# Kernel tuning notes

Hardware: AMD Instinct MI355X
Metric: run time of the kernel (lower is better)

## Reference

```python
import jax, jax.numpy as jnp
import numpy as np

N_HEAD = 16
LN_EPS = 1e-5


def _layernorm(x, g, b):
    mu = jnp.mean(x, axis=-1, keepdims=True)
    var = jnp.var(x, axis=-1, keepdims=True)
    return (x - mu) * jax.lax.rsqrt(var + LN_EPS) * g + b


def setup_inputs() -> dict:
    key = jax.random.key(0)
    ks = jax.random.split(key, 8)
    B, T, C = 8, 1024, 1024
    s = lambda fan_in: 1.0 / np.sqrt(fan_in)
    return {
        "x": jax.random.normal(ks[0], (B, T, C), jnp.float32),
        "kqv_w": jax.random.normal(ks[1], (3 * C, C), jnp.float32) * s(C),
        "kqv_b": jnp.zeros((3 * C,), jnp.float32),
        "proj_w": jax.random.normal(ks[2], (C, C), jnp.float32) * s(C),
        "proj_b": jnp.zeros((C,), jnp.float32),
        "ln1_g": jnp.ones((C,), jnp.float32),
        "ln1_b": jnp.zeros((C,), jnp.float32),
        "ln2_g": jnp.ones((C,), jnp.float32),
        "ln2_b": jnp.zeros((C,), jnp.float32),
        "fc1_w": jax.random.normal(ks[3], (4 * C, C), jnp.float32) * s(C),
        "fc1_b": jnp.zeros((4 * C,), jnp.float32),
        "fc2_w": jax.random.normal(ks[4], (C, 4 * C), jnp.float32) * s(4 * C),
        "fc2_b": jnp.zeros((C,), jnp.float32),
    }


def reference(x, kqv_w, kqv_b, proj_w, proj_b, ln1_g, ln1_b, ln2_g, ln2_b,
              fc1_w, fc1_b, fc2_w, fc2_b):
    B, T, C = x.shape
    hd = C // N_HEAD

    # --- attention sublayer ---
    h = _layernorm(x, ln1_g, ln1_b)
    kqv = h @ kqv_w.T + kqv_b                     # [B,T,3C]
    kqv = kqv.reshape(B, T, N_HEAD, 3 * hd)
    # ts.slice(kqv, 3, dim=-1) -> (k, q, v) in that order
    k = kqv[..., 0 * hd:1 * hd].transpose(0, 2, 1, 3)  # [B,H,T,hd]
    q = kqv[..., 1 * hd:2 * hd].transpose(0, 2, 1, 3)
    v = kqv[..., 2 * hd:3 * hd].transpose(0, 2, 1, 3)

    att = jnp.einsum('bhqd,bhkd->bhqk', q, k) * (1.0 / np.sqrt(hd))
    causal = jnp.tril(jnp.ones((T, T), dtype=bool))
    att = jnp.where(causal, att, jnp.float32(-jnp.inf))
    att = jax.nn.softmax(att, axis=-1)
    y = jnp.einsum('bhqk,bhkd->bhqd', att, v)     # [B,H,T,hd]
    y = y.transpose(0, 2, 1, 3).reshape(B, T, C)
    x = x + (y @ proj_w.T + proj_b)

    # --- MLP sublayer ---
    h = _layernorm(x, ln2_g, ln2_b)
    h = jax.nn.gelu(h @ fc1_w.T + fc1_b, approximate=False)  # nn.GELU exact
    x = x + (h @ fc2_w.T + fc2_b)
    return x
```

## Files before the change

### kernel.cpp

```cpp
#include <hip/hip_runtime.h>
#include <math.h>
#include <stdint.h>

typedef __bf16 bf16_t;
typedef __bf16 bf16x8 __attribute__((ext_vector_type(8)));
typedef float f32x4 __attribute__((ext_vector_type(4)));
typedef unsigned short ushort8_t __attribute__((ext_vector_type(8)));
typedef unsigned short ushort4_t __attribute__((ext_vector_type(4)));

#define LOG2E 1.44269504088896340736f

__device__ inline unsigned short f2bf_bits(float f) {
  union { float f; unsigned int u; } v; v.f = f;
  unsigned int u = v.u;
  return (unsigned short)((u + 0x7fffu + ((u >> 16) & 1u)) >> 16);
}

__device__ inline void gld_lds16(const void* g, void* l) {
  __builtin_amdgcn_global_load_lds(
      (__attribute__((address_space(1))) void*)(uintptr_t)(g),
      (__attribute__((address_space(3))) void*)(uintptr_t)(l),
      16, 0, 0);
}

#define BAR() __builtin_amdgcn_s_barrier()
#define LGKM0() asm volatile("s_waitcnt lgkmcnt(0)" ::: "memory")
#define VMW(n) asm volatile("s_waitcnt vmcnt(" #n ")" ::: "memory")
#define PRIO(p) __builtin_amdgcn_s_setprio(p)

__global__ __launch_bounds__(256) void cast_kernel(const float* __restrict__ in,
                                                   unsigned short* __restrict__ out,
                                                   int n) {
  int i = (blockIdx.x * 256 + threadIdx.x) * 4;
  if (i >= n) return;
  float4 f = *reinterpret_cast<const float4*>(in + i);
  ushort4_t o;
  o[0] = f2bf_bits(f.x); o[1] = f2bf_bits(f.y);
  o[2] = f2bf_bits(f.z); o[3] = f2bf_bits(f.w);
  *reinterpret_cast<ushort4_t*>(out + i) = o;
}

__global__ __launch_bounds__(256) void ln_kernel(const float* __restrict__ x,
                                                 const float* __restrict__ g,
                                                 const float* __restrict__ bta,
                                                 unsigned short* __restrict__ out) {
  const int row = blockIdx.x;
  const int c = threadIdx.x * 4;
  const float4 xv = *reinterpret_cast<const float4*>(x + (size_t)row * 1024 + c);
  float s = xv.x + xv.y + xv.z + xv.w;
  float sq = xv.x * xv.x + xv.y * xv.y + xv.z * xv.z + xv.w * xv.w;
#pragma unroll
  for (int xm = 1; xm < 64; xm <<= 1) {
    s += __shfl_xor(s, xm, 64);
    sq += __shfl_xor(sq, xm, 64);
  }
  __shared__ float sh[8];
  const int wave = threadIdx.x >> 6, lane = threadIdx.x & 63;
  if (lane == 0) { sh[wave] = s; sh[4 + wave] = sq; }
  __syncthreads();
  const float ts = sh[0] + sh[1] + sh[2] + sh[3];
  const float tq = sh[4] + sh[5] + sh[6] + sh[7];
  const float mean = ts * (1.0f / 1024.0f);
  const float var = tq * (1.0f / 1024.0f) - mean * mean;
  const float rstd = rsqrtf(var + 1e-5f);
  const float4 gv = *reinterpret_cast<const float4*>(g + c);
  const float4 bv = *reinterpret_cast<const float4*>(bta + c);
  ushort4_t o;
  o[0] = f2bf_bits((xv.x - mean) * rstd * gv.x + bv.x);
  o[1] = f2bf_bits((xv.y - mean) * rstd * gv.y + bv.y);
  o[2] = f2bf_bits((xv.z - mean) * rstd * gv.z + bv.z);
  o[3] = f2bf_bits((xv.w - mean) * rstd * gv.w + bv.w);
  *reinterpret_cast<ushort4_t*>(out + (size_t)row * 1024 + c) = o;
}

#define LDAF(SLOT)                                                            \
  do {                                                                        \
    _Pragma("unroll") for (int mi_ = 0; mi_ < 4; ++mi_)                       \
    _Pragma("unroll") for (int kh_ = 0; kh_ < 2; ++kh_) {                     \
      const int row_ = wm * 64 + mi_ * 16 + lr16;                             \
      af[mi_][kh_] = *reinterpret_cast<const bf16x8*>(                        \
          &lds[(SLOT) * AS + row_ * 64 + ((kh_ * 32 + lk * 8) ^ axor)]);      \
    }                                                                         \
  } while (0)

#define LDBF(SLOT, HALF)                                                      \
  do {                                                                        \
    _Pragma("unroll") for (int n2_ = 0; n2_ < 2; ++n2_)                       \
    _Pragma("unroll") for (int kh_ = 0; kh_ < 2; ++kh_) {                     \
      const int row_ = wn * 64 + ((HALF) * 2 + n2_) * 16 + lr16;              \
      bf[n2_][kh_] = *reinterpret_cast<const bf16x8*>(                        \
          &lds[BS0 + (SLOT) * BSS + row_ * 64 + ((kh_ * 32 + lk * 8) ^ axor)]); \
    }                                                                         \
  } while (0)

#define PMMA(HALF)                                                            \
  do {                                                                        \
    _Pragma("unroll") for (int mi_ = 0; mi_ < 4; ++mi_)                       \
    _Pragma("unroll") for (int n2_ = 0; n2_ < 2; ++n2_)                       \
    _Pragma("unroll") for (int kh_ = 0; kh_ < 2; ++kh_)                       \
      acc[mi_][(HALF) * 2 + n2_] = __builtin_amdgcn_mfma_f32_16x16x32_bf16(   \
          af[mi_][kh_], bf[n2_][kh_], acc[mi_][(HALF) * 2 + n2_], 0, 0, 0);   \
  } while (0)

template <int EPI>
__global__ __launch_bounds__(512) void gemm8(const unsigned short* __restrict__ A,
                                             const unsigned short* __restrict__ W,
                                             const float* __restrict__ bias,
                                             const float* __restrict__ res,
                                             unsigned short* __restrict__ outb,
                                             float* __restrict__ outf,
                                             int N, int K) {
  __shared__ unsigned short lds[(2 * 128 + 2 * 256) * 64];
  const int tid = threadIdx.x;
  const int w = tid >> 6, l = tid & 63;
  const int m0 = blockIdx.y * 128, n0 = blockIdx.x * 256;
  const int wm = w >> 2, wn = w & 3;
  const int lr16 = l & 15, lk = l >> 4;
  const int axor = (lr16 & 7) << 3;

  const int AS = 128 * 64;
  const int BS0 = 2 * 128 * 64;
  const int BSS = 256 * 64;

  const int sr = tid >> 3;
  const int sx = ((tid & 7) ^ (sr & 7)) << 3;
  auto stA = [&](int t, int h) {
    gld_lds16(A + (size_t)(m0 + h * 64 + sr) * K + t * 64 + sx,
              &lds[(t & 1) * AS + h * 4096 + tid * 8]);
  };
  auto stB = [&](int t, int c) {
    gld_lds16(W + (size_t)(n0 + c * 64 + sr) * K + t * 64 + sx,
              &lds[BS0 + (t & 1) * BSS + c * 4096 + tid * 8]);
  };

  f32x4 acc[4][4];
#pragma unroll
  for (int i = 0; i < 4; ++i)
#pragma unroll
    for (int j = 0; j < 4; ++j) { f32x4 z = {0.f, 0.f, 0.f, 0.f}; acc[i][j] = z; }
  bf16x8 af[4][2], bf[2][2];

  stA(0, 0); stA(0, 1);
  stB(0, 0); stB(0, 1); stB(0, 2); stB(0, 3);
  stA(1, 0); stA(1, 1);
  VMW(2);
  BAR();

  const int nt = K / 64;
  for (int e = 0; e < nt; e += 2) {
    const int o = e + 1;
    const int e2 = (e + 2 < nt) ? (e + 2) : 0;
    const int o2 = (e + 3 < nt) ? (e + 3) : 1;

    LDAF(0); LDBF(0, 0);
    stB(o, 0); stB(o, 1); stB(o, 2); stB(o, 3);
    BAR(); LGKM0(); PRIO(1); PMMA(0); PRIO(0); BAR();
    LDBF(0, 1);
    stA(e2, 0); stA(e2, 1);
    BAR(); LGKM0(); PRIO(1); PMMA(1); PRIO(0);
    VMW(2);
    BAR();
    LDAF(1); LDBF(1, 0);
    stB(e2, 0); stB(e2, 1); stB(e2, 2); stB(e2, 3);
    BAR(); LGKM0(); PRIO(1); PMMA(0); PRIO(0); BAR();
    LDBF(1, 1);
    stA(o2, 0); stA(o2, 1);
    BAR(); LGKM0(); PRIO(1); PMMA(1); PRIO(0);
    VMW(2);
    BAR();
  }
  VMW(0);

#pragma unroll
  for (int ni = 0; ni < 4; ++ni) {
    const int col = n0 + wn * 64 + ni * 16 + lr16;
    const float bv = bias[col];
#pragma unroll
    for (int mi = 0; mi < 4; ++mi) {
#pragma unroll
      for (int r = 0; r < 4; ++r) {
        const int row = m0 + wm * 64 + mi * 16 + lk * 4 + r;
        const size_t idx = (size_t)row * N + col;
        float v = acc[mi][ni][r] + bv;
        if (EPI == 0) {
          outb[idx] = f2bf_bits(v);
        } else if (EPI == 1) {
          outf[idx] = v + res[idx];
        } else {
          v = 0.5f * v * (1.0f + erff(v * 0.70710678118654752f));
          outb[idx] = f2bf_bits(v);
        }
      }
    }
  }
}

__device__ inline int swz(int row, int colelem) {
  return row * 64 + (colelem ^ ((row & 7) << 3));
}

__global__ __launch_bounds__(256) void attn_kernel(const unsigned short* __restrict__ kqv,
                                                   unsigned short* __restrict__ y) {
  __shared__ unsigned short Ks[2][64 * 64];
  __shared__ unsigned short Vt[2][64 * 64];
  __shared__ unsigned short Ps[4][16 * 64];

  const int tid = threadIdx.x;
  const int wave = tid >> 6;
  const int lane = tid & 63;
  const int bh = blockIdx.x;
  const int pair = blockIdx.y;
  const int b = bh >> 4;
  const int h = bh & 15;
  const int lo = pair;
  const int hi = 15 - pair;
  const int bT = b * 1024;
  const int hoff = h * 192;

  auto loadq = [&](int q0t, bf16x8 (&qf)[2]) {
    const unsigned short* qp =
        kqv + (size_t)(bT + q0t + wave * 16 + (lane & 15)) * 3072 + hoff + 64 +
        (lane >> 4) * 8;
#pragma unroll
    for (int kk = 0; kk < 2; ++kk) {
      bf16x8 t = *reinterpret_cast<const bf16x8*>(qp + kk * 32);
#pragma unroll
      for (int e = 0; e < 8; ++e) t[e] = (bf16_t)((float)t[e] * 0.125f);
      qf[kk] = t;
    }
  };

  auto stageK = [&](int j0, int bufi) {
#pragma unroll
    for (int i = 0; i < 2; ++i) {
      const int off = i * 4096 + wave * 1024 + lane * 16;
      const int jr = off >> 7;
      const int ce = ((off & 127) >> 1) ^ ((jr & 7) << 3);
      gld_lds16(kqv + (size_t)(bT + j0 + jr) * 3072 + hoff + ce,
                &Ks[bufi][i * 2048 + wave * 512]);
    }
  };

  ushort8_t vreg0, vreg1;
  auto vload = [&](int j0) {
    const unsigned short* vp =
        kqv + (size_t)(bT + j0 + (tid & 63)) * 3072 + hoff + 128 + (tid >> 6) * 8;
    vreg0 = *reinterpret_cast<const ushort8_t*>(vp);
    vreg1 = *reinterpret_cast<const ushort8_t*>(vp + 32);
  };
  auto vwrite = [&](int bufi) {
    const int j = tid & 63;
    const int dg = tid >> 6;
#pragma unroll
    for (int e = 0; e < 8; ++e) Vt[bufi][swz(dg * 8 + e, j)] = vreg0[e];
#pragma unroll
    for (int e = 0; e < 8; ++e) Vt[bufi][swz((dg + 4) * 8 + e, j)] = vreg1[e];
  };

  auto compute = [&](const bf16x8 (&qf)[2], f32x4 (&acc_o)[4], float (&mr)[4],
                     float (&lr)[4], int q0t, int j0, bool diag, int cur) {
    f32x4 s[4];
#pragma unroll
    for (int nt = 0; nt < 4; ++nt) {
      f32x4 a = {0.f, 0.f, 0.f, 0.f};
#pragma unroll
      for (int kk = 0; kk < 2; ++kk) {
        const bf16x8 kf = *reinterpret_cast<const bf16x8*>(
            &Ks[cur][swz(nt * 16 + (lane & 15), kk * 32 + (lane >> 4) * 8)]);
        a = __builtin_amdgcn_mfma_f32_16x16x32_bf16(qf[kk], kf, a, 0, 0, 0);
      }
      s[nt] = a;
    }
#pragma unroll
    for (int r = 0; r < 4; ++r) {
      float mx = -1e30f;
      if (diag) {
        const int qg = q0t + wave * 16 + ((lane >> 4) << 2) + r;
#pragma unroll
        for (int nt = 0; nt < 4; ++nt) {
          const int jg = j0 + nt * 16 + (lane & 15);
          const float sv = (jg <= qg) ? s[nt][r] : -1e30f;
          s[nt][r] = sv;
          mx = fmaxf(mx, sv);
        }
      } else {
#pragma unroll
        for (int nt = 0; nt < 4; ++nt) mx = fmaxf(mx, s[nt][r]);
      }
#pragma unroll
      for (int xm = 1; xm < 16; xm <<= 1) mx = fmaxf(mx, __shfl_xor(mx, xm, 64));
      const float mnew = fmaxf(mr[r], mx);
      const float sc = exp2f((mr[r] - mnew) * LOG2E);
      mr[r] = mnew;
      float ssum = 0.f;
#pragma unroll
      for (int nt = 0; nt < 4; ++nt) {
        const float p = exp2f((s[nt][r] - mnew) * LOG2E);
        s[nt][r] = p;
        ssum += p;
      }
#pragma unroll
      for (int xm = 1; xm < 16; xm <<= 1) ssum += __shfl_xor(ssum, xm, 64);
      lr[r] = lr[r] * sc + ssum;
#pragma unroll
      for (int dt = 0; dt < 4; ++dt) acc_o[dt][r] *= sc;
    }
    unsigned short* Pw = &Ps[wave][0];
#pragma unroll
    for (int nt = 0; nt < 4; ++nt)
#pragma unroll
      for (int r = 0; r < 4; ++r)
        Pw[swz(((lane >> 4) << 2) + r, nt * 16 + (lane & 15))] = f2bf_bits(s[nt][r]);
#pragma unroll
    for (int kk = 0; kk < 2; ++kk) {
      const bf16x8 pf = *reinterpret_cast<const bf16x8*>(
          &Ps[wave][swz(lane & 15, kk * 32 + (lane >> 4) * 8)]);
#pragma unroll
      for (int dt = 0; dt < 4; ++dt) {
        const bf16x8 vf = *reinterpret_cast<const bf16x8*>(
            &Vt[cur][swz(dt * 16 + (lane & 15), kk * 32 + (lane >> 4) * 8)]);
        acc_o[dt] = __builtin_amdgcn_mfma_f32_16x16x32_bf16(pf, vf, acc_o[dt], 0, 0, 0);
      }
    }
  };

  auto writeo = [&](int q0t, f32x4 (&acc_o)[4], float (&lr)[4]) {
#pragma unroll
    for (int dt = 0; dt < 4; ++dt)
#pragma unroll
      for (int r = 0; r < 4; ++r) {
        const int qg = q0t + wave * 16 + ((lane >> 4) << 2) + r;
        y[(size_t)(bT + qg) * 1024 + h * 64 + dt * 16 + (lane & 15)] =
            f2bf_bits(acc_o[dt][r] / lr[r]);
      }
  };

  bf16x8 qf_l[2], qf_h[2];
  loadq(lo * 64, qf_l);
  loadq(hi * 64, qf_h);
  f32x4 acc_l[4], acc_h[4];
#pragma unroll
  for (int dt = 0; dt < 4; ++dt) {
    f32x4 z = {0.f, 0.f, 0.f, 0.f};
    acc_l[dt] = z;
    acc_h[dt] = z;
  }
  float mr_l[4] = {-1e30f, -1e30f, -1e30f, -1e30f};
  float mr_h[4] = {-1e30f, -1e30f, -1e30f, -1e30f};
  float lr_l[4] = {0.f, 0.f, 0.f, 0.f};
  float lr_h[4] = {0.f, 0.f, 0.f, 0.f};

  stageK(0, 0);
  vload(0);
  vwrite(0);

  for (int jt = 0; jt <= hi; ++jt) {
    const int cur = jt & 1;
    __syncthreads();
    if (jt < hi) {
      stageK((jt + 1) * 64, cur ^ 1);
      vload((jt + 1) * 64);
    }
    compute(qf_h, acc_h, mr_h, lr_h, hi * 64, jt * 64, jt == hi, cur);
    if (jt <= lo)
      compute(qf_l, acc_l, mr_l, lr_l, lo * 64, jt * 64, jt == lo, cur);
    if (jt < hi) vwrite(cur ^ 1);
  }

  writeo(hi * 64, acc_h, lr_h);
  writeo(lo * 64, acc_l, lr_l);
}

extern "C" void kernel_launch(void* const* d_in, const int* in_sizes, int n_in,
                              void* d_out, int out_size, void* d_ws, size_t ws_size,
                              hipStream_t stream) {
  const float* x = (const float*)d_in[0];
  const float* kqv_w = (const float*)d_in[1];
  const float* kqv_b = (const float*)d_in[2];
  const float* proj_w = (const float*)d_in[3];
  const float* proj_b = (const float*)d_in[4];
  const float* ln1_g = (const float*)d_in[5];
  const float* ln1_b = (const float*)d_in[6];
  const float* ln2_g = (const float*)d_in[7];
  const float* ln2_b = (const float*)d_in[8];
  const float* fc1_w = (const float*)d_in[9];
  const float* fc1_b = (const float*)d_in[10];
  const float* fc2_w = (const float*)d_in[11];
  const float* fc2_b = (const float*)d_in[12];
  float* out = (float*)d_out;

  char* ws = (char*)d_ws;
  size_t off = 0;
  auto alloc = [&](size_t bytes) {
    char* p = ws + off;
    off += (bytes + 255) & ~(size_t)255;
    return p;
  };
  unsigned short* wk = (unsigned short*)alloc((size_t)3072 * 1024 * 2);
  unsigned short* wp = (unsigned short*)alloc((size_t)1024 * 1024 * 2);
  unsigned short* w1 = (unsigned short*)alloc((size_t)4096 * 1024 * 2);
  unsigned short* w2 = (unsigned short*)alloc((size_t)4096 * 1024 * 2);
  unsigned short* hbuf = (unsigned short*)alloc((size_t)8192 * 1024 * 2);
  unsigned short* kqvb = (unsigned short*)alloc((size_t)8192 * 3072 * 2);
  unsigned short* yb = (unsigned short*)alloc((size_t)8192 * 1024 * 2);
  float* x1 = (float*)alloc((size_t)8192 * 1024 * 4);
  unsigned short* a1 = (unsigned short*)alloc((size_t)8192 * 4096 * 2);

  cast_kernel<<<dim3(3072 * 1024 / 1024), 256, 0, stream>>>(kqv_w, wk, 3072 * 1024);
  cast_kernel<<<dim3(1024 * 1024 / 1024), 256, 0, stream>>>(proj_w, wp, 1024 * 1024);
  cast_kernel<<<dim3(4096 * 1024 / 1024), 256, 0, stream>>>(fc1_w, w1, 4096 * 1024);
  cast_kernel<<<dim3(4096 * 1024 / 1024), 256, 0, stream>>>(fc2_w, w2, 4096 * 1024);

  ln_kernel<<<dim3(8192), 256, 0, stream>>>(x, ln1_g, ln1_b, hbuf);

  gemm8<0><<<dim3(3072 / 256, 8192 / 128), 512, 0, stream>>>(
      hbuf, wk, kqv_b, nullptr, kqvb, nullptr, 3072, 1024);

  attn_kernel<<<dim3(128, 8), 256, 0, stream>>>(kqvb, yb);

  gemm8<1><<<dim3(1024 / 256, 8192 / 128), 512, 0, stream>>>(
      yb, wp, proj_b, x, nullptr, x1, 1024, 1024);

  ln_kernel<<<dim3(8192), 256, 0, stream>>>(x1, ln2_g, ln2_b, hbuf);

  gemm8<2><<<dim3(4096 / 256, 8192 / 128), 512, 0, stream>>>(
      hbuf, w1, fc1_b, nullptr, a1, nullptr, 4096, 1024);

  gemm8<1><<<dim3(1024 / 256, 8192 / 128), 512, 0, stream>>>(
      a1, w2, fc2_b, x1, nullptr, out, 1024, 4096);
}
```

Before: 445.5 us.

## Triple-buffer GEMM LDS tiles to prefetch two K-steps ahead

Converts the bf16 GEMM main loop from a double-buffered, two-step unrolled schedule to a three-slot LDS ring that issues global-to-LDS loads two tiles ahead. Loads stay in flight longer before the wait, which is meant to hide global memory latency behind the MFMA work. LDS use grows from 96KB to 144KB per block, and the loop now ends with explicit epilogue iterations. The larger LDS footprint could limit occupancy, and the loop is no longer unrolled by two.

```diff
diff --git a/kernel.cpp b/kernel.cpp
--- a/kernel.cpp
+++ b/kernel.cpp
@@ -73,23 +73,23 @@
   *reinterpret_cast<ushort4_t*>(out + (size_t)row * 1024 + c) = o;
 }
 
-#define LDAF(SLOT)                                                            \
+#define LDAF(SL)                                                              \
   do {                                                                        \
     _Pragma("unroll") for (int mi_ = 0; mi_ < 4; ++mi_)                       \
     _Pragma("unroll") for (int kh_ = 0; kh_ < 2; ++kh_) {                     \
       const int row_ = wm * 64 + mi_ * 16 + lr16;                             \
       af[mi_][kh_] = *reinterpret_cast<const bf16x8*>(                        \
-          &lds[(SLOT) * AS + row_ * 64 + ((kh_ * 32 + lk * 8) ^ axor)]);      \
+          &lds[(SL) * ASLOT + row_ * 64 + ((kh_ * 32 + lk * 8) ^ axor)]);     \
     }                                                                         \
   } while (0)
 
-#define LDBF(SLOT, HALF)                                                      \
+#define LDBF(SL, HALF)                                                        \
   do {                                                                        \
     _Pragma("unroll") for (int n2_ = 0; n2_ < 2; ++n2_)                       \
     _Pragma("unroll") for (int kh_ = 0; kh_ < 2; ++kh_) {                     \
       const int row_ = wn * 64 + ((HALF) * 2 + n2_) * 16 + lr16;              \
       bf[n2_][kh_] = *reinterpret_cast<const bf16x8*>(                        \
-          &lds[BS0 + (SLOT) * BSS + row_ * 64 + ((kh_ * 32 + lk * 8) ^ axor)]); \
+          &lds[B0 + (SL) * BSLOT + row_ * 64 + ((kh_ * 32 + lk * 8) ^ axor)]); \
     }                                                                         \
   } while (0)
 
@@ -110,7 +110,7 @@
                                              unsigned short* __restrict__ outb,
                                              float* __restrict__ outf,
                                              int N, int K) {
-  __shared__ unsigned short lds[(2 * 128 + 2 * 256) * 64];
+  __shared__ unsigned short lds[3 * (128 + 256) * 64];
   const int tid = threadIdx.x;
   const int w = tid >> 6, l = tid & 63;
   const int m0 = blockIdx.y * 128, n0 = blockIdx.x * 256;
@@ -118,19 +118,19 @@
   const int lr16 = l & 15, lk = l >> 4;
   const int axor = (lr16 & 7) << 3;
 
-  const int AS = 128 * 64;
-  const int BS0 = 2 * 128 * 64;
-  const int BSS = 256 * 64;
+  const int ASLOT = 128 * 64;
+  const int B0 = 3 * ASLOT;
+  const int BSLOT = 256 * 64;
 
   const int sr = tid >> 3;
   const int sx = ((tid & 7) ^ (sr & 7)) << 3;
-  auto stA = [&](int t, int h) {
+  auto stA = [&](int t, int s, int h) {
     gld_lds16(A + (size_t)(m0 + h * 64 + sr) * K + t * 64 + sx,
-              &lds[(t & 1) * AS + h * 4096 + tid * 8]);
-  };
-  auto stB = [&](int t, int c) {
+              &lds[s * ASLOT + h * 4096 + tid * 8]);
+  };
+  auto stB = [&](int t, int s, int c) {
     gld_lds16(W + (size_t)(n0 + c * 64 + sr) * K + t * 64 + sx,
-              &lds[BS0 + (t & 1) * BSS + c * 4096 + tid * 8]);
+              &lds[B0 + s * BSLOT + c * 4096 + tid * 8]);
   };
 
   f32x4 acc[4][4];
@@ -140,36 +140,41 @@
     for (int j = 0; j < 4; ++j) { f32x4 z = {0.f, 0.f, 0.f, 0.f}; acc[i][j] = z; }
   bf16x8 af[4][2], bf[2][2];
 
-  stA(0, 0); stA(0, 1);
-  stB(0, 0); stB(0, 1); stB(0, 2); stB(0, 3);
-  stA(1, 0); stA(1, 1);
-  VMW(2);
+  stA(0, 0, 0); stA(0, 0, 1);
+  stB(0, 0, 0); stB(0, 0, 1); stB(0, 0, 2); stB(0, 0, 3);
+  stA(1, 1, 0); stA(1, 1, 1);
+  stB(1, 1, 0); stB(1, 1, 1); stB(1, 1, 2); stB(1, 1, 3);
+  VMW(6);
   BAR();
 
   const int nt = K / 64;
-  for (int e = 0; e < nt; e += 2) {
-    const int o = e + 1;
-    const int e2 = (e + 2 < nt) ? (e + 2) : 0;
-    const int o2 = (e + 3 < nt) ? (e + 3) : 1;
-
-    LDAF(0); LDBF(0, 0);
-    stB(o, 0); stB(o, 1); stB(o, 2); stB(o, 3);
+  int s = 0;
+  int sp = 2;
+  for (int t = 0; t < nt - 2; ++t) {
+    const int tp2 = t + 2;
+    LDAF(s); LDBF(s, 0);
+    stA(tp2, sp, 0); stA(tp2, sp, 1);
+    stB(tp2, sp, 0); stB(tp2, sp, 1);
     BAR(); LGKM0(); PRIO(1); PMMA(0); PRIO(0); BAR();
-    LDBF(0, 1);
-    stA(e2, 0); stA(e2, 1);
+    LDBF(s, 1);
+    stB(tp2, sp, 2); stB(tp2, sp, 3);
     BAR(); LGKM0(); PRIO(1); PMMA(1); PRIO(0);
-    VMW(2);
+    VMW(6);
     BAR();
-    LDAF(1); LDBF(1, 0);
-    stB(e2, 0); stB(e2, 1); stB(e2, 2); stB(e2, 3);
-    BAR(); LGKM0(); PRIO(1); PMMA(0); PRIO(0); BAR();
-    LDBF(1, 1);
-    stA(o2, 0); stA(o2, 1);
-    BAR(); LGKM0(); PRIO(1); PMMA(1); PRIO(0);
-    VMW(2);
-    BAR();
+    s = (s == 2) ? 0 : s + 1;
+    sp = (sp == 2) ? 0 : sp + 1;
   }
+  LDAF(s); LDBF(s, 0);
+  BAR(); LGKM0(); PRIO(1); PMMA(0); PRIO(0); BAR();
+  LDBF(s, 1);
+  BAR(); LGKM0(); PRIO(1); PMMA(1); PRIO(0);
   VMW(0);
+  BAR();
+  s = (s == 2) ? 0 : s + 1;
+  LDAF(s); LDBF(s, 0);
+  BAR(); LGKM0(); PRIO(1); PMMA(0); PRIO(0); BAR();
+  LDBF(s, 1);
+  LGKM0(); PRIO(1); PMMA(1); PRIO(0);
 
 #pragma unroll
   for (int ni = 0; ni < 4; ++ni) {
```

Result: no change. 445.6 us (+0.0%).
